# Performance work log

Measured on AMD Instinct MI355X. Metric: run time of the kernel, lower is better.

The kernel has to match this reference:

```python
import jax, jax.numpy as jnp
import numpy as np

D_MODEL = 1024
ADAPT = 128
NUM_LIB = 8
BATCH = 1024


def setup_inputs() -> dict:
    key = jax.random.key(0)
    k_x, k_src, k_tgt, k_w1, k_w2 = jax.random.split(key, 5)
    hidden_states = jax.random.normal(k_x, (BATCH, D_MODEL), dtype=jnp.float32)
    source_library = jax.random.randint(k_src, (BATCH,), 0, NUM_LIB, dtype=jnp.int32)
    target_library = jax.random.randint(k_tgt, (BATCH,), 0, NUM_LIB, dtype=jnp.int32)
    # Stacked translator weights: slot p = src*NUM_LIB + tgt. Diagonal slots
    # (src==tgt) exist for uniform indexing but are masked out (identity path).
    P = NUM_LIB * NUM_LIB
    s1 = 1.0 / np.sqrt(D_MODEL).astype(np.float32)
    s2 = 1.0 / np.sqrt(ADAPT).astype(np.float32)
    W1 = jax.random.normal(k_w1, (P, D_MODEL, ADAPT), dtype=jnp.float32) * s1
    b1 = jnp.zeros((P, ADAPT), dtype=jnp.float32)
    W2 = jax.random.normal(k_w2, (P, ADAPT, D_MODEL), dtype=jnp.float32) * s2
    b2 = jnp.zeros((P, D_MODEL), dtype=jnp.float32)
    return {
        "hidden_states": hidden_states,
        "source_library": source_library,
        "target_library": target_library,
        "W1": W1, "b1": b1, "W2": W2, "b2": b2,
    }


def reference(hidden_states, source_library, target_library, W1, b1, W2, b2):
    # L recovered from stacked expert table [L*L, d, a]
    L = int(np.sqrt(W1.shape[0]))
    pair = source_library * L + target_library  # [B]
    # Per-sample expert weights (grouped-GEMM formulation of the python loop)
    h = jax.nn.relu(jnp.einsum('bd,bda->ba', hidden_states, W1[pair]) + b1[pair])
    y = jnp.einsum('ba,bad->bd', h, W2[pair]) + b2[pair]
    # src == tgt -> identity (original appends hidden_states[i] unchanged)
    same = (source_library == target_library)[:, None]
    return jnp.where(same, hidden_states, y)
```

## Files before the change

kernel.cpp:

```cpp
#include <hip/hip_runtime.h>

#define D_MODEL 1024
#define ADAPT   128
#define NUM_LIB 8
#define BATCH   1024
#define CH      16
#define NSLOT   128

typedef __attribute__((ext_vector_type(8))) short bf16x8;
typedef __attribute__((ext_vector_type(4))) float f32x4;

__device__ __forceinline__ short f2bf(float f) {
  unsigned u = __float_as_uint(f);
  u += 0x7FFFu + ((u >> 16) & 1u);
  return (short)(u >> 16);
}

__global__ __launch_bounds__(1024) void bucket_k(const int* __restrict__ src,
                                                 const int* __restrict__ tgt,
                                                 int* __restrict__ perm,
                                                 int* __restrict__ cpair,
                                                 int* __restrict__ cbase,
                                                 int* __restrict__ cm) {
  __shared__ int cnt[64];
  __shared__ int offs[64];
  __shared__ int pos[64];
  int t = threadIdx.x;
  if (t < 64) { cnt[t] = 0; pos[t] = 0; }
  __syncthreads();
  int pair = src[t] * NUM_LIB + tgt[t];
  atomicAdd(&cnt[pair], 1);
  __syncthreads();
  if (t == 0) {
    int acc = 0;
    for (int i = 0; i < 64; i++) { offs[i] = acc; acc += cnt[i]; }
  }
  __syncthreads();
  int sl = atomicAdd(&pos[pair], 1);
  perm[offs[pair] + sl] = t;
  if (t == 0) {
    int nc = 0;
    for (int p = 0; p < 64; p++) {
      for (int c0 = 0; c0 < cnt[p]; c0 += CH) {
        cpair[nc] = p;
        cbase[nc] = offs[p] + c0;
        cm[nc]    = min(CH, cnt[p] - c0);
        nc++;
      }
    }
    for (; nc < NSLOT; nc++) cpair[nc] = -1;
  }
}

#define XS_STR 1032
#define WT_STR 136

__global__ __launch_bounds__(256) void gemm1_k(const float* __restrict__ x,
                                               const float* __restrict__ W1,
                                               const float* __restrict__ b1,
                                               const int* __restrict__ perm,
                                               const int* __restrict__ cpair,
                                               const int* __restrict__ cbase,
                                               const int* __restrict__ cm,
                                               float* __restrict__ H) {
  int slot = blockIdx.x;
  int p = cpair[slot];
  if (p < 0 || (p % 9) == 0) return;
  int m    = cm[slot];
  int base = cbase[slot];
  int a0   = blockIdx.y * 64;
  __shared__ int   rows_s[CH];
  __shared__ short xs[CH * XS_STR];
  __shared__ short wt[64 * WT_STR];
  int t = threadIdx.x;
  if (t < CH) rows_s[t] = perm[base + min(t, m - 1)];
  __syncthreads();
  {
    int s = t & 15, jg = t >> 4;
    const float* xr = x + (size_t)rows_s[s] * D_MODEL + jg * 64;
    short* xw = xs + s * XS_STR + jg * 64;
#pragma unroll
    for (int i = 0; i < 16; i++) {
      float4 v = *(const float4*)(xr + i * 4);
      short4 o;
      o.x = f2bf(v.x); o.y = f2bf(v.y); o.z = f2bf(v.z); o.w = f2bf(v.w);
      *(short4*)(xw + i * 4) = o;
    }
  }
  int lane = t & 63;
  int wvid = t >> 6;
  int col  = lane & 15;
  int quad = lane >> 4;
  f32x4 acc = {0.f, 0.f, 0.f, 0.f};
  int a_st = t & 63, kg = t >> 6;
  for (int k0 = 0; k0 < D_MODEL; k0 += 128) {
    {
      const float* wr = W1 + ((size_t)p * D_MODEL + k0 + kg * 32) * ADAPT + a0 + a_st;
      short* ww = wt + a_st * WT_STR + kg * 32;
#pragma unroll
      for (int ii = 0; ii < 4; ii++) {
        bf16x8 o;
#pragma unroll
        for (int i = 0; i < 8; i++) o[i] = f2bf(wr[(ii * 8 + i) * ADAPT]);
        *(bf16x8*)(ww + ii * 8) = o;
      }
    }
    __syncthreads();
#pragma unroll
    for (int kk = 0; kk < 4; kk++) {
      bf16x8 af = *(const bf16x8*)(xs + col * XS_STR + k0 + kk * 32 + quad * 8);
      bf16x8 bv = *(const bf16x8*)(wt + (wvid * 16 + col) * WT_STR + kk * 32 + quad * 8);
      acc = __builtin_amdgcn_mfma_f32_16x16x32_bf16(af, bv, acc, 0, 0, 0);
    }
    __syncthreads();
  }
  int a = a0 + wvid * 16 + col;
  float bb = b1[p * ADAPT + a];
#pragma unroll
  for (int r = 0; r < 4; r++) {
    int s = quad * 4 + r;
    if (s < m) H[(size_t)rows_s[s] * ADAPT + a] = fmaxf(acc[r] + bb, 0.f);
  }
}

#define HS_STR  136
#define WT2_STR 136

__global__ __launch_bounds__(256) void gemm2_k(const float* __restrict__ x,
                                               const float* __restrict__ W2,
                                               const float* __restrict__ b2,
                                               const int* __restrict__ perm,
                                               const int* __restrict__ cpair,
                                               const int* __restrict__ cbase,
                                               const int* __restrict__ cm,
                                               const float* __restrict__ H,
                                               float* __restrict__ out) {
  int slot = blockIdx.x;
  int p = cpair[slot];
  if (p < 0) return;
  int m    = cm[slot];
  int base = cbase[slot];
  int d0   = blockIdx.y * 128;
  __shared__ int rows_s[CH];
  int t = threadIdx.x;
  if (t < CH) rows_s[t] = perm[base + min(t, m - 1)];
  __syncthreads();
  if ((p % 9) == 0) {
    int s = t >> 4, j = t & 15;
    if (s < m) {
      size_t off = (size_t)rows_s[s] * D_MODEL + d0 + j * 8;
      float4 v0 = *(const float4*)(x + off);
      float4 v1 = *(const float4*)(x + off + 4);
      *(float4*)(out + off)     = v0;
      *(float4*)(out + off + 4) = v1;
    }
    return;
  }
  __shared__ short hs[CH * HS_STR];
  __shared__ short wt[128 * WT2_STR];
  {
    int s = t & 15, j = t >> 4;
    const float* hr = H + (size_t)rows_s[s] * ADAPT + j * 8;
    float4 v0 = *(const float4*)hr;
    float4 v1 = *(const float4*)(hr + 4);
    bf16x8 o;
    o[0] = f2bf(v0.x); o[1] = f2bf(v0.y); o[2] = f2bf(v0.z); o[3] = f2bf(v0.w);
    o[4] = f2bf(v1.x); o[5] = f2bf(v1.y); o[6] = f2bf(v1.z); o[7] = f2bf(v1.w);
    *(bf16x8*)(hs + s * HS_STR + j * 8) = o;
  }
  {
    int dl = t & 127, half = t >> 7;
#pragma unroll
    for (int kgi = 0; kgi < 8; kgi++) {
      int kb = kgi * 16 + half * 8;
      const float* wr = W2 + ((size_t)p * ADAPT + kb) * D_MODEL + d0 + dl;
      bf16x8 o;
#pragma unroll
      for (int i = 0; i < 8; i++) o[i] = f2bf(wr[i * D_MODEL]);
      *(bf16x8*)(wt + dl * WT2_STR + kb) = o;
    }
  }
  __syncthreads();
  int lane = t & 63, wvid = t >> 6, col = lane & 15, quad = lane >> 4;
  f32x4 acc0 = {0.f, 0.f, 0.f, 0.f};
  f32x4 acc1 = {0.f, 0.f, 0.f, 0.f};
#pragma unroll
  for (int kk = 0; kk < 4; kk++) {
    bf16x8 af = *(const bf16x8*)(hs + col * HS_STR + kk * 32 + quad * 8);
    bf16x8 b0 = *(const bf16x8*)(wt + (wvid * 32 + col) * WT2_STR + kk * 32 + quad * 8);
    bf16x8 b1v = *(const bf16x8*)(wt + (wvid * 32 + 16 + col) * WT2_STR + kk * 32 + quad * 8);
    acc0 = __builtin_amdgcn_mfma_f32_16x16x32_bf16(af, b0, acc0, 0, 0, 0);
    acc1 = __builtin_amdgcn_mfma_f32_16x16x32_bf16(af, b1v, acc1, 0, 0, 0);
  }
  int d_a = d0 + wvid * 32 + col;
  int d_b = d_a + 16;
  float bba = b2[(size_t)p * D_MODEL + d_a];
  float bbb = b2[(size_t)p * D_MODEL + d_b];
#pragma unroll
  for (int r = 0; r < 4; r++) {
    int s = quad * 4 + r;
    if (s < m) {
      size_t ro = (size_t)rows_s[s] * D_MODEL;
      out[ro + d_a] = acc0[r] + bba;
      out[ro + d_b] = acc1[r] + bbb;
    }
  }
}

extern "C" void kernel_launch(void* const* d_in, const int* in_sizes, int n_in,
                              void* d_out, int out_size, void* d_ws, size_t ws_size,
                              hipStream_t stream) {
  const float* x   = (const float*)d_in[0];
  const int*   src = (const int*)d_in[1];
  const int*   tgt = (const int*)d_in[2];
  const float* W1  = (const float*)d_in[3];
  const float* b1  = (const float*)d_in[4];
  const float* W2  = (const float*)d_in[5];
  const float* b2  = (const float*)d_in[6];
  float* out = (float*)d_out;

  float* H    = (float*)d_ws;
  int* perm   = (int*)(H + (size_t)BATCH * ADAPT);
  int* cpair  = perm + BATCH;
  int* cbase  = cpair + NSLOT;
  int* cmarr  = cbase + NSLOT;

  bucket_k<<<1, 1024, 0, stream>>>(src, tgt, perm, cpair, cbase, cmarr);
  gemm1_k<<<dim3(NSLOT, 2), 256, 0, stream>>>(x, W1, b1, perm, cpair, cbase, cmarr, H);
  gemm2_k<<<dim3(NSLOT, 8), 256, 0, stream>>>(x, W2, b2, perm, cpair, cbase, cmarr, H, out);
  (void)in_sizes; (void)n_in; (void)out_size; (void)ws_size;
}
```

Measured before the change: 139.9 us.

## Split GEMM1 K-dimension across blocks and parallelize bucket slot table build

The first GEMM now splits its reduction over D_MODEL into two halves along a new grid z dimension. Each half writes a partial H into its own workspace buffer, and the second GEMM sums the partials and applies bias plus ReLU as it loads H. K tiles grow to 256 so each block loops twice instead of eight times, which doubles the block count and halves the per-block serial W1 streaming. The bucketing kernel also builds its chunk table with 64 threads using precomputed chunk offsets instead of one serial thread. The cost is an extra H buffer, more global traffic for H, and larger shared tiles that may lower occupancy.

```diff
diff --git a/kernel.cpp b/kernel.cpp
--- a/kernel.cpp
+++ b/kernel.cpp
@@ -25,6 +25,7 @@
   __shared__ int cnt[64];
   __shared__ int offs[64];
   __shared__ int pos[64];
+  __shared__ int choff[65];
   int t = threadIdx.x;
   if (t < 64) { cnt[t] = 0; pos[t] = 0; }
   __syncthreads();
@@ -32,43 +33,47 @@
   atomicAdd(&cnt[pair], 1);
   __syncthreads();
   if (t == 0) {
-    int acc = 0;
-    for (int i = 0; i < 64; i++) { offs[i] = acc; acc += cnt[i]; }
+    int acc = 0, ch = 0;
+    for (int i = 0; i < 64; i++) {
+      offs[i] = acc; acc += cnt[i];
+      choff[i] = ch; ch += (cnt[i] + CH - 1) / CH;
+    }
+    choff[64] = ch;
   }
   __syncthreads();
   int sl = atomicAdd(&pos[pair], 1);
   perm[offs[pair] + sl] = t;
-  if (t == 0) {
-    int nc = 0;
-    for (int p = 0; p < 64; p++) {
-      for (int c0 = 0; c0 < cnt[p]; c0 += CH) {
-        cpair[nc] = p;
-        cbase[nc] = offs[p] + c0;
-        cm[nc]    = min(CH, cnt[p] - c0);
-        nc++;
-      }
-    }
-    for (; nc < NSLOT; nc++) cpair[nc] = -1;
-  }
-}
-
-#define XS_STR 1032
-#define WT_STR 136
+  if (t < 64) {
+    int nc = (cnt[t] + CH - 1) / CH, c0 = choff[t];
+    for (int c = 0; c < nc; c++) {
+      cpair[c0 + c] = t;
+      cbase[c0 + c] = offs[t] + c * CH;
+      cm[c0 + c]    = min(CH, cnt[t] - c * CH);
+    }
+  } else if (t < 64 + NSLOT) {
+    int slotid = t - 64;
+    if (slotid >= choff[64]) cpair[slotid] = -1;
+  }
+}
+
+#define BK     256
+#define XS_STR 520
+#define WT_STR 264
 
 __global__ __launch_bounds__(256) void gemm1_k(const float* __restrict__ x,
                                                const float* __restrict__ W1,
-                                               const float* __restrict__ b1,
                                                const int* __restrict__ perm,
                                                const int* __restrict__ cpair,
                                                const int* __restrict__ cbase,
                                                const int* __restrict__ cm,
-                                               float* __restrict__ H) {
+                                               float* __restrict__ Hp) {
   int slot = blockIdx.x;
   int p = cpair[slot];
   if (p < 0 || (p % 9) == 0) return;
   int m    = cm[slot];
   int base = cbase[slot];
   int a0   = blockIdx.y * 64;
+  int kh   = blockIdx.z;
   __shared__ int   rows_s[CH];
   __shared__ short xs[CH * XS_STR];
   __shared__ short wt[64 * WT_STR];
@@ -77,28 +82,25 @@
   __syncthreads();
   {
     int s = t & 15, jg = t >> 4;
-    const float* xr = x + (size_t)rows_s[s] * D_MODEL + jg * 64;
-    short* xw = xs + s * XS_STR + jg * 64;
-#pragma unroll
-    for (int i = 0; i < 16; i++) {
+    const float* xr = x + (size_t)rows_s[s] * D_MODEL + kh * 512 + jg * 32;
+    short* xw = xs + s * XS_STR + jg * 32;
+#pragma unroll
+    for (int i = 0; i < 8; i++) {
       float4 v = *(const float4*)(xr + i * 4);
       short4 o;
       o.x = f2bf(v.x); o.y = f2bf(v.y); o.z = f2bf(v.z); o.w = f2bf(v.w);
       *(short4*)(xw + i * 4) = o;
     }
   }
-  int lane = t & 63;
-  int wvid = t >> 6;
-  int col  = lane & 15;
-  int quad = lane >> 4;
+  int lane = t & 63, wvid = t >> 6, col = lane & 15, quad = lane >> 4;
   f32x4 acc = {0.f, 0.f, 0.f, 0.f};
   int a_st = t & 63, kg = t >> 6;
-  for (int k0 = 0; k0 < D_MODEL; k0 += 128) {
+  for (int r = 0; r < 2; r++) {
     {
-      const float* wr = W1 + ((size_t)p * D_MODEL + k0 + kg * 32) * ADAPT + a0 + a_st;
-      short* ww = wt + a_st * WT_STR + kg * 32;
-#pragma unroll
-      for (int ii = 0; ii < 4; ii++) {
+      const float* wr = W1 + ((size_t)p * D_MODEL + kh * 512 + r * BK + kg * 64) * ADAPT + a0 + a_st;
+      short* ww = wt + a_st * WT_STR + kg * 64;
+#pragma unroll
+      for (int ii = 0; ii < 8; ii++) {
         bf16x8 o;
 #pragma unroll
         for (int i = 0; i < 8; i++) o[i] = f2bf(wr[(ii * 8 + i) * ADAPT]);
@@ -107,19 +109,19 @@
     }
     __syncthreads();
 #pragma unroll
-    for (int kk = 0; kk < 4; kk++) {
-      bf16x8 af = *(const bf16x8*)(xs + col * XS_STR + k0 + kk * 32 + quad * 8);
+    for (int kk = 0; kk < 8; kk++) {
+      bf16x8 af = *(const bf16x8*)(xs + col * XS_STR + r * BK + kk * 32 + quad * 8);
       bf16x8 bv = *(const bf16x8*)(wt + (wvid * 16 + col) * WT_STR + kk * 32 + quad * 8);
       acc = __builtin_amdgcn_mfma_f32_16x16x32_bf16(af, bv, acc, 0, 0, 0);
     }
     __syncthreads();
   }
   int a = a0 + wvid * 16 + col;
-  float bb = b1[p * ADAPT + a];
+  float* Hb = Hp + (size_t)kh * BATCH * ADAPT;
 #pragma unroll
   for (int r = 0; r < 4; r++) {
     int s = quad * 4 + r;
-    if (s < m) H[(size_t)rows_s[s] * ADAPT + a] = fmaxf(acc[r] + bb, 0.f);
+    if (s < m) Hb[(size_t)rows_s[s] * ADAPT + a] = acc[r];
   }
 }
 
@@ -128,12 +130,13 @@
 
 __global__ __launch_bounds__(256) void gemm2_k(const float* __restrict__ x,
                                                const float* __restrict__ W2,
+                                               const float* __restrict__ b1,
                                                const float* __restrict__ b2,
                                                const int* __restrict__ perm,
                                                const int* __restrict__ cpair,
                                                const int* __restrict__ cbase,
                                                const int* __restrict__ cm,
-                                               const float* __restrict__ H,
+                                               const float* __restrict__ Hp,
                                                float* __restrict__ out) {
   int slot = blockIdx.x;
   int p = cpair[slot];
@@ -160,12 +163,13 @@
   __shared__ short wt[128 * WT2_STR];
   {
     int s = t & 15, j = t >> 4;
-    const float* hr = H + (size_t)rows_s[s] * ADAPT + j * 8;
-    float4 v0 = *(const float4*)hr;
-    float4 v1 = *(const float4*)(hr + 4);
+    size_t ho = (size_t)rows_s[s] * ADAPT + j * 8;
+    const float* h0 = Hp + ho;
+    const float* h1 = Hp + (size_t)BATCH * ADAPT + ho;
+    const float* bb = b1 + (size_t)p * ADAPT + j * 8;
     bf16x8 o;
-    o[0] = f2bf(v0.x); o[1] = f2bf(v0.y); o[2] = f2bf(v0.z); o[3] = f2bf(v0.w);
-    o[4] = f2bf(v1.x); o[5] = f2bf(v1.y); o[6] = f2bf(v1.z); o[7] = f2bf(v1.w);
+#pragma unroll
+    for (int i = 0; i < 8; i++) o[i] = f2bf(fmaxf(h0[i] + h1[i] + bb[i], 0.f));
     *(bf16x8*)(hs + s * HS_STR + j * 8) = o;
   }
   {
@@ -219,14 +223,14 @@
   const float* b2  = (const float*)d_in[6];
   float* out = (float*)d_out;
 
-  float* H    = (float*)d_ws;
-  int* perm   = (int*)(H + (size_t)BATCH * ADAPT);
+  float* Hp   = (float*)d_ws;
+  int* perm   = (int*)(Hp + 2 * (size_t)BATCH * ADAPT);
   int* cpair  = perm + BATCH;
   int* cbase  = cpair + NSLOT;
   int* cmarr  = cbase + NSLOT;
 
   bucket_k<<<1, 1024, 0, stream>>>(src, tgt, perm, cpair, cbase, cmarr);
-  gemm1_k<<<dim3(NSLOT, 2), 256, 0, stream>>>(x, W1, b1, perm, cpair, cbase, cmarr, H);
-  gemm2_k<<<dim3(NSLOT, 8), 256, 0, stream>>>(x, W2, b2, perm, cpair, cbase, cmarr, H, out);
+  gemm1_k<<<dim3(NSLOT, 2, 2), 256, 0, stream>>>(x, W1, perm, cpair, cbase, cmarr, Hp);
+  gemm2_k<<<dim3(NSLOT, 8), 256, 0, stream>>>(x, W2, b1, b2, perm, cpair, cbase, cmarr, Hp, out);
   (void)in_sizes; (void)n_in; (void)out_size; (void)ws_size;
 }
```

Result: faster. 126.4 us (-9.7%).
